# Kernel tuning notes

Hardware: AMD Instinct MI355X
Metric: run time of the kernel (lower is better)

The kernel has to match this reference:

```python
import jax, jax.numpy as jnp
import numpy as np

B, T, IN, H, L, OUT = 1024, 48, 64, 512, 3, 1


def setup_inputs() -> dict:
    key = jax.random.key(0)
    ks = jax.random.split(key, 12)
    s = 0.05
    inp = {
        "x": jax.random.normal(ks[0], (B, T, IN), dtype=jnp.float32),
        # layer 0: input IN -> H ; gates concatenated [f,i,c,o] along last dim
        "Wx0": jax.random.normal(ks[1], (IN, 4 * H), dtype=jnp.float32) * s,
        "Wh0": jax.random.normal(ks[2], (H, 4 * H), dtype=jnp.float32) * s,
        "b0": jnp.zeros((4 * H,), dtype=jnp.float32),
        "Wx1": jax.random.normal(ks[3], (H, 4 * H), dtype=jnp.float32) * s,
        "Wh1": jax.random.normal(ks[4], (H, 4 * H), dtype=jnp.float32) * s,
        "b1": jnp.zeros((4 * H,), dtype=jnp.float32),
        "Wx2": jax.random.normal(ks[5], (H, 4 * H), dtype=jnp.float32) * s,
        "Wh2": jax.random.normal(ks[6], (H, 4 * H), dtype=jnp.float32) * s,
        "b2": jnp.zeros((4 * H,), dtype=jnp.float32),
        "fc_w": jax.random.normal(ks[7], (H, OUT), dtype=jnp.float32) * s,
        "fc_b": jnp.zeros((OUT,), dtype=jnp.float32),
    }
    return inp


def _lstm_cell(Wx, Wh, b, x_t, h, C):
    # fused 4-gate GEMM, same math as 8 separate Linears in the torch code
    g = x_t @ Wx + h @ Wh + b  # [B, 4H]
    f, i, c, o = jnp.split(g, 4, axis=-1)
    f = jax.nn.sigmoid(f)
    i = jax.nn.sigmoid(i)
    c = jnp.tanh(c)
    o = jax.nn.sigmoid(o)
    C_new = f * C + i * c
    h_new = o * jnp.tanh(C_new)  # dropout is identity in eval mode
    return h_new, C_new


def reference(x, Wx0, Wh0, b0, Wx1, Wh1, b1, Wx2, Wh2, b2, fc_w, fc_b):
    params = [(Wx0, Wh0, b0), (Wx1, Wh1, b1), (Wx2, Wh2, b2)]
    Bsz = x.shape[0]
    Hsz = Wh0.shape[0]
    h0 = jnp.zeros((L, Bsz, Hsz), dtype=x.dtype)
    C0 = jnp.zeros((L, Bsz, Hsz), dtype=x.dtype)

    def step(carry, x_t):
        h, C = carry
        inp = x_t
        hs, Cs = [], []
        for l in range(L):
            Wx, Wh, b = params[l]
            hn, Cn = _lstm_cell(Wx, Wh, b, inp, h[l], C[l])
            hs.append(hn)
            Cs.append(Cn)
            inp = hn
        return (jnp.stack(hs), jnp.stack(Cs)), None

    (h, C), _ = jax.lax.scan(step, (h0, C0), jnp.swapaxes(x, 0, 1))
    return h[-1] @ fc_w + fc_b  # [B, OUT]
```

## Files before the change

kernel.cpp:

```cpp
#include <hip/hip_runtime.h>
#include <hip/hip_bf16.h>
#include <stdint.h>

#define BSZ 1024
#define HSZ 512
#define TSZ 48
#define INSZ 64
#define GSZ 2048

typedef __attribute__((ext_vector_type(8))) short bf16x8;
typedef __attribute__((ext_vector_type(4))) float f32x4;

#define GLDS16(g, l)                                                        \
    __builtin_amdgcn_global_load_lds(                                       \
        (const __attribute__((address_space(1))) void*)(g),                 \
        (__attribute__((address_space(3))) void*)(l), 16, 0, 0)

__device__ __forceinline__ float sigmf(float x) { return 1.0f / (1.0f + __expf(-x)); }
__device__ __forceinline__ float tanhf_(float x) { return 2.0f / (1.0f + __expf(-2.0f * x)) - 1.0f; }

__global__ __launch_bounds__(256, 3) void lstm_diag(
    const __hip_bfloat16* __restrict__ xth, const __hip_bfloat16* __restrict__ xtl,
    __hip_bfloat16* __restrict__ hbuf,
    float* __restrict__ Cbuf,
    const __hip_bfloat16* __restrict__ W0h, const __hip_bfloat16* __restrict__ W0l,
    const __hip_bfloat16* __restrict__ W1h, const __hip_bfloat16* __restrict__ W1l,
    const __hip_bfloat16* __restrict__ W2h, const __hip_bfloat16* __restrict__ W2l,
    const float* __restrict__ b0, const float* __restrict__ b1,
    const float* __restrict__ b2,
    int d, int lmin)
{
    __shared__ __align__(16) char lds[49152];

    const int l = lmin + blockIdx.z;
    const int t = d - l;
    const size_t slab = (size_t)BSZ * HSZ;
    __hip_bfloat16* hb = hbuf;
    auto Hb = [&](int par, int ll, int hilo) {
        return hb + (((size_t)par * 3 + ll) * 2 + hilo) * slab;
    };

    const __hip_bfloat16* Wth = (l == 0) ? W0h : (l == 1) ? W1h : W2h;
    const __hip_bfloat16* Wtl = (l == 0) ? W0l : (l == 1) ? W1l : W2l;
    const float* bias = (l == 0) ? b0 : (l == 1) ? b1 : b2;
    const int Kx   = (l == 0) ? INSZ : HSZ;
    const int Ktot = Kx + HSZ;
    const int cur = t & 1, prv = cur ^ 1;
    const __hip_bfloat16* Axh = (l == 0) ? xth + (size_t)t * BSZ * INSZ : Hb(cur, l - 1, 0);
    const __hip_bfloat16* Axl = (l == 0) ? xtl + (size_t)t * BSZ * INSZ : Hb(cur, l - 1, 1);
    const int ldax = Kx;
    const __hip_bfloat16* Ahh = Hb(prv, l, 0);
    const __hip_bfloat16* Ahl = Hb(prv, l, 1);
    float* C = Cbuf + (size_t)l * slab;
    __hip_bfloat16* hhi = Hb(cur, l, 0);
    __hip_bfloat16* hlo = Hb(cur, l, 1);

    const int bid = blockIdx.x + (blockIdx.y << 4);
    const int swz = (bid & 7) * 32 + (bid >> 3);
    const int m0 = (swz & 15) * 64;
    const int n0 = (swz >> 4) * 128;

    const int tid = threadIdx.x;
    const int lane = tid & 63;
    const int wv = tid >> 6;
    const int lrow = lane & 15;
    const int lk = lane >> 4;

    int offA[4][2], offB[2][2];
#pragma unroll
    for (int m = 0; m < 4; ++m) {
        int row = m * 16 + lrow;
#pragma unroll
        for (int kk = 0; kk < 2; ++kk)
            offA[m][kk] = (row * 128 + (lk + kk * 4) * 16) ^ ((row & 7) << 4);
    }
#pragma unroll
    for (int j = 0; j < 2; ++j) {
        int n = wv * 32 + j * 16 + lrow;
#pragma unroll
        for (int kk = 0; kk < 2; ++kk)
            offB[j][kk] = (n * 128 + (lk + kk * 4) * 16) ^ ((n & 7) << 4);
    }

    int rowA[2], ksA[2];
#pragma unroll
    for (int i = 0; i < 2; ++i) {
        int seg = (wv * 2 + i) * 64 + lane;
        rowA[i] = seg >> 3;
        ksA[i] = ((seg & 7) ^ (rowA[i] & 7)) * 8;
    }
    int rowB[4], ksB[4];
#pragma unroll
    for (int i = 0; i < 4; ++i) {
        int seg = (wv * 4 + i) * 64 + lane;
        rowB[i] = seg >> 3;
        ksB[i] = ((seg & 7) ^ (rowB[i] & 7)) * 8;
    }

    char* ldsAh = lds;
    char* ldsAl = lds + 8192;
    char* ldsBh = lds + 16384;
    char* ldsBl = lds + 32768;

    f32x4 acc[4][2];
#pragma unroll
    for (int m = 0; m < 4; ++m)
#pragma unroll
        for (int j = 0; j < 2; ++j) acc[m][j] = (f32x4){0.f, 0.f, 0.f, 0.f};

    auto kstep = [&](const __hip_bfloat16* Ah_, const __hip_bfloat16* Al_, int ldA,
                     int kA, int kW) {
        __syncthreads();
#pragma unroll
        for (int i = 0; i < 2; ++i) {
            size_t ro = (size_t)(m0 + rowA[i]) * ldA + kA + ksA[i];
            GLDS16(Ah_ + ro, ldsAh + (wv * 2 + i) * 1024);
            GLDS16(Al_ + ro, ldsAl + (wv * 2 + i) * 1024);
        }
#pragma unroll
        for (int i = 0; i < 4; ++i) {
            size_t ro = (size_t)(n0 + rowB[i]) * Ktot + kW + ksB[i];
            GLDS16(Wth + ro, ldsBh + (wv * 4 + i) * 1024);
            GLDS16(Wtl + ro, ldsBl + (wv * 4 + i) * 1024);
        }
        __syncthreads();
#pragma unroll
        for (int kk = 0; kk < 2; ++kk) {
            bf16x8 a_h[4], a_l[4], b_h[2], b_l[2];
#pragma unroll
            for (int m = 0; m < 4; ++m) {
                a_h[m] = *(const bf16x8*)(ldsAh + offA[m][kk]);
                a_l[m] = *(const bf16x8*)(ldsAl + offA[m][kk]);
            }
#pragma unroll
            for (int j = 0; j < 2; ++j) {
                b_h[j] = *(const bf16x8*)(ldsBh + offB[j][kk]);
                b_l[j] = *(const bf16x8*)(ldsBl + offB[j][kk]);
            }
#pragma unroll
            for (int m = 0; m < 4; ++m)
#pragma unroll
                for (int j = 0; j < 2; ++j) {
                    acc[m][j] = __builtin_amdgcn_mfma_f32_16x16x32_bf16(a_h[m], b_h[j], acc[m][j], 0, 0, 0);
                    acc[m][j] = __builtin_amdgcn_mfma_f32_16x16x32_bf16(a_l[m], b_h[j], acc[m][j], 0, 0, 0);
                    acc[m][j] = __builtin_amdgcn_mfma_f32_16x16x32_bf16(a_h[m], b_l[j], acc[m][j], 0, 0, 0);
                }
        }
    };

#pragma unroll 1
    for (int k0 = 0; k0 < Kx; k0 += 64) kstep(Axh, Axl, ldax, k0, k0);
#pragma unroll 1
    for (int k0 = 0; k0 < HSZ; k0 += 64) kstep(Ahh, Ahl, HSZ, k0, Kx + k0);

    __syncthreads();
    float* gt = (float*)lds;
#pragma unroll
    for (int m = 0; m < 4; ++m)
#pragma unroll
        for (int j = 0; j < 2; ++j) {
            int col = wv * 32 + j * 16 + lrow;
            int rb = m * 16 + lk * 4;
#pragma unroll
            for (int r = 0; r < 4; ++r) gt[(rb + r) * 132 + col] = acc[m][j][r];
        }
    __syncthreads();

    const int n_l = tid & 31;
    const int rb2 = (tid >> 5) * 8;
    const int n_g = (n0 >> 2) + n_l;
    const float bf = bias[n_g], bi = bias[HSZ + n_g];
    const float bc = bias[2 * HSZ + n_g], bo = bias[3 * HSZ + n_g];
#pragma unroll
    for (int r = 0; r < 8; ++r) {
        int row = rb2 + r;
        int rg = m0 + row;
        float4 g4 = *(const float4*)&gt[row * 132 + n_l * 4];
        float f = sigmf(g4.x + bf);
        float i_ = sigmf(g4.y + bi);
        float c_ = tanhf_(g4.z + bc);
        float o_ = sigmf(g4.w + bo);
        size_t idx = (size_t)rg * HSZ + n_g;
        float Cn = f * C[idx] + i_ * c_;
        C[idx] = Cn;
        float hv = o_ * tanhf_(Cn);
        __hip_bfloat16 hh = __float2bfloat16(hv);
        hhi[idx] = hh;
        hlo[idx] = __float2bfloat16(hv - __bfloat162float(hh));
    }
}

__global__ __launch_bounds__(256) void convert_x(const float* __restrict__ x,
                                                 __hip_bfloat16* __restrict__ xh,
                                                 __hip_bfloat16* __restrict__ xl)
{
    int idx = blockIdx.x * 256 + threadIdx.x;
    int i4 = idx & 15;
    int bt = idx >> 4;
    int t = bt % TSZ;
    int b = bt / TSZ;
    float4 v = *(const float4*)(x + ((size_t)b * TSZ + t) * INSZ + i4 * 4);
    size_t o = ((size_t)t * BSZ + b) * INSZ + i4 * 4;
    float vv[4] = {v.x, v.y, v.z, v.w};
#pragma unroll
    for (int j = 0; j < 4; ++j) {
        __hip_bfloat16 h = __float2bfloat16(vv[j]);
        xh[o + j] = h;
        xl[o + j] = __float2bfloat16(vv[j] - __bfloat162float(h));
    }
}

__global__ __launch_bounds__(256) void convert_w(
    const float* __restrict__ Wx, const float* __restrict__ Wh, int Kx, int Ktot,
    __hip_bfloat16* __restrict__ outh, __hip_bfloat16* __restrict__ outl)
{
    __shared__ float tile[64][65];
    int k0 = blockIdx.x * 64;
    int c0 = blockIdx.y * 64;
    int nb = c0 >> 2;
    const float* src;
    int krel;
    if (k0 < Kx) { src = Wx; krel = k0; } else { src = Wh; krel = k0 - Kx; }
#pragma unroll
    for (int i = 0; i < 16; ++i) {
        int idx = threadIdx.x + i * 256;
        int k_l = idx >> 6, c_l = idx & 63;
        int g = c_l >> 4, n_l = c_l & 15;
        tile[k_l][n_l * 4 + g] = src[(size_t)(krel + k_l) * GSZ + g * HSZ + nb + n_l];
    }
    __syncthreads();
#pragma unroll
    for (int i = 0; i < 16; ++i) {
        int idx = threadIdx.x + i * 256;
        int r_l = idx >> 6, k_l = idx & 63;
        float v = tile[k_l][r_l];
        __hip_bfloat16 h = __float2bfloat16(v);
        size_t o = (size_t)(c0 + r_l) * Ktot + k0 + k_l;
        outh[o] = h;
        outl[o] = __float2bfloat16(v - __bfloat162float(h));
    }
}

__global__ __launch_bounds__(256) void fc_kernel(
    const __hip_bfloat16* __restrict__ hh, const __hip_bfloat16* __restrict__ hl,
    const float* __restrict__ w, const float* __restrict__ b, float* __restrict__ out)
{
    int wave = (blockIdx.x * 256 + threadIdx.x) >> 6;
    int lane = threadIdx.x & 63;
    if (wave >= BSZ) return;
    float s = 0.0f;
#pragma unroll
    for (int k = lane; k < HSZ; k += 64)
        s += (__bfloat162float(hh[wave * HSZ + k]) + __bfloat162float(hl[wave * HSZ + k])) * w[k];
#pragma unroll
    for (int off = 32; off; off >>= 1) s += __shfl_down(s, off);
    if (lane == 0) out[wave] = s + b[0];
}

extern "C" void kernel_launch(void* const* d_in, const int* in_sizes, int n_in,
                              void* d_out, int out_size, void* d_ws, size_t ws_size,
                              hipStream_t stream) {
    const float* x   = (const float*)d_in[0];
    const float* Wx0 = (const float*)d_in[1];
    const float* Wh0 = (const float*)d_in[2];
    const float* b0  = (const float*)d_in[3];
    const float* Wx1 = (const float*)d_in[4];
    const float* Wh1 = (const float*)d_in[5];
    const float* b1  = (const float*)d_in[6];
    const float* Wx2 = (const float*)d_in[7];
    const float* Wh2 = (const float*)d_in[8];
    const float* b2  = (const float*)d_in[9];
    const float* fcw = (const float*)d_in[10];
    const float* fcb = (const float*)d_in[11];

    char* p = (char*)d_ws;
    const size_t hslab = (size_t)BSZ * HSZ * sizeof(__hip_bfloat16);
    __hip_bfloat16* hbuf = (__hip_bfloat16*)p;
    p += 12 * hslab;
    float* Cbuf = (float*)p;
    p += 3 * (size_t)BSZ * HSZ * sizeof(float);
    const size_t zero_bytes = (size_t)(p - (char*)d_ws);

    const size_t xslab = (size_t)TSZ * BSZ * INSZ * sizeof(__hip_bfloat16);
    __hip_bfloat16* xth = (__hip_bfloat16*)p; p += xslab;
    __hip_bfloat16* xtl = (__hip_bfloat16*)p; p += xslab;

    const int K0 = INSZ + HSZ;
    const int K12 = 2 * HSZ;
    const size_t w0s = (size_t)GSZ * K0 * sizeof(__hip_bfloat16);
    const size_t w12s = (size_t)GSZ * K12 * sizeof(__hip_bfloat16);
    __hip_bfloat16* w0h = (__hip_bfloat16*)p; p += w0s;
    __hip_bfloat16* w0l = (__hip_bfloat16*)p; p += w0s;
    __hip_bfloat16* w1h = (__hip_bfloat16*)p; p += w12s;
    __hip_bfloat16* w1l = (__hip_bfloat16*)p; p += w12s;
    __hip_bfloat16* w2h = (__hip_bfloat16*)p; p += w12s;
    __hip_bfloat16* w2l = (__hip_bfloat16*)p; p += w12s;

    hipMemsetAsync(d_ws, 0, zero_bytes, stream);

    convert_x<<<dim3(BSZ * TSZ * 16 / 256), dim3(256), 0, stream>>>(x, xth, xtl);
    convert_w<<<dim3(K0 / 64, GSZ / 64), dim3(256), 0, stream>>>(Wx0, Wh0, INSZ, K0, w0h, w0l);
    convert_w<<<dim3(K12 / 64, GSZ / 64), dim3(256), 0, stream>>>(Wx1, Wh1, HSZ, K12, w1h, w1l);
    convert_w<<<dim3(K12 / 64, GSZ / 64), dim3(256), 0, stream>>>(Wx2, Wh2, HSZ, K12, w2h, w2l);

    for (int dgn = 0; dgn < TSZ + 2; ++dgn) {
        int lmin = (dgn - (TSZ - 1)) > 0 ? (dgn - (TSZ - 1)) : 0;
        int lmax = dgn < 2 ? dgn : 2;
        int ncells = lmax - lmin + 1;
        lstm_diag<<<dim3(16, 16, ncells), dim3(256), 0, stream>>>(
            xth, xtl, hbuf, Cbuf,
            w0h, w0l, w1h, w1l, w2h, w2l,
            b0, b1, b2, dgn, lmin);
    }

    __hip_bfloat16* h2h = hbuf + (((size_t)1 * 3 + 2) * 2 + 0) * BSZ * HSZ;
    __hip_bfloat16* h2l = hbuf + (((size_t)1 * 3 + 2) * 2 + 1) * BSZ * HSZ;
    fc_kernel<<<dim3(BSZ / 4), dim3(256), 0, stream>>>(h2h, h2l, fcw, fcb, (float*)d_out);
}
```

Before: 1.869 ms.

## Double-buffer activation tiles in LDS and load weights directly into registers

```diff
diff --git a/kernel.cpp b/kernel.cpp
--- a/kernel.cpp
+++ b/kernel.cpp
@@ -30,14 +30,13 @@
     const float* __restrict__ b2,
     int d, int lmin)
 {
-    __shared__ __align__(16) char lds[49152];
+    __shared__ __align__(16) char lds[33792];
 
     const int l = lmin + blockIdx.z;
     const int t = d - l;
     const size_t slab = (size_t)BSZ * HSZ;
-    __hip_bfloat16* hb = hbuf;
     auto Hb = [&](int par, int ll, int hilo) {
-        return hb + (((size_t)par * 3 + ll) * 2 + hilo) * slab;
+        return hbuf + (((size_t)par * 3 + ll) * 2 + hilo) * slab;
     };
 
     const __hip_bfloat16* Wth = (l == 0) ? W0h : (l == 1) ? W1h : W2h;
@@ -45,10 +44,11 @@
     const float* bias = (l == 0) ? b0 : (l == 1) ? b1 : b2;
     const int Kx   = (l == 0) ? INSZ : HSZ;
     const int Ktot = Kx + HSZ;
+    const int nkx  = Kx >> 6;
+    const int nkt  = Ktot >> 6;
     const int cur = t & 1, prv = cur ^ 1;
     const __hip_bfloat16* Axh = (l == 0) ? xth + (size_t)t * BSZ * INSZ : Hb(cur, l - 1, 0);
     const __hip_bfloat16* Axl = (l == 0) ? xtl + (size_t)t * BSZ * INSZ : Hb(cur, l - 1, 1);
-    const int ldax = Kx;
     const __hip_bfloat16* Ahh = Hb(prv, l, 0);
     const __hip_bfloat16* Ahl = Hb(prv, l, 1);
     float* C = Cbuf + (size_t)l * slab;
@@ -66,20 +66,13 @@
     const int lrow = lane & 15;
     const int lk = lane >> 4;
 
-    int offA[4][2], offB[2][2];
+    int offA[4][2];
 #pragma unroll
     for (int m = 0; m < 4; ++m) {
         int row = m * 16 + lrow;
 #pragma unroll
         for (int kk = 0; kk < 2; ++kk)
             offA[m][kk] = (row * 128 + (lk + kk * 4) * 16) ^ ((row & 7) << 4);
-    }
-#pragma unroll
-    for (int j = 0; j < 2; ++j) {
-        int n = wv * 32 + j * 16 + lrow;
-#pragma unroll
-        for (int kk = 0; kk < 2; ++kk)
-            offB[j][kk] = (n * 128 + (lk + kk * 4) * 16) ^ ((n & 7) << 4);
     }
 
     int rowA[2], ksA[2];
@@ -89,18 +82,11 @@
         rowA[i] = seg >> 3;
         ksA[i] = ((seg & 7) ^ (rowA[i] & 7)) * 8;
     }
-    int rowB[4], ksB[4];
-#pragma unroll
-    for (int i = 0; i < 4; ++i) {
-        int seg = (wv * 4 + i) * 64 + lane;
-        rowB[i] = seg >> 3;
-        ksB[i] = ((seg & 7) ^ (rowB[i] & 7)) * 8;
-    }
-
-    char* ldsAh = lds;
-    char* ldsAl = lds + 8192;
-    char* ldsBh = lds + 16384;
-    char* ldsBl = lds + 32768;
+
+    const int bcol = n0 + wv * 32 + lrow;
+    const __hip_bfloat16* pB0h = Wth + (size_t)bcol * Ktot + lk * 8;
+    const __hip_bfloat16* pB0l = Wtl + (size_t)bcol * Ktot + lk * 8;
+    const size_t jstride = (size_t)16 * Ktot;
 
     f32x4 acc[4][2];
 #pragma unroll
@@ -108,52 +94,65 @@
 #pragma unroll
         for (int j = 0; j < 2; ++j) acc[m][j] = (f32x4){0.f, 0.f, 0.f, 0.f};
 
-    auto kstep = [&](const __hip_bfloat16* Ah_, const __hip_bfloat16* Al_, int ldA,
-                     int kA, int kW) {
-        __syncthreads();
+    auto stage = [&](int ks, int buf) {
+        const __hip_bfloat16* sh;
+        const __hip_bfloat16* sl;
+        int ldA, krel;
+        if (ks < nkx) { sh = Axh; sl = Axl; ldA = Kx; krel = ks * 64; }
+        else          { sh = Ahh; sl = Ahl; ldA = HSZ; krel = (ks - nkx) * 64; }
+        char* dh = lds + buf * 16384;
+        char* dl = dh + 8192;
 #pragma unroll
         for (int i = 0; i < 2; ++i) {
-            size_t ro = (size_t)(m0 + rowA[i]) * ldA + kA + ksA[i];
-            GLDS16(Ah_ + ro, ldsAh + (wv * 2 + i) * 1024);
-            GLDS16(Al_ + ro, ldsAl + (wv * 2 + i) * 1024);
+            size_t ro = (size_t)(m0 + rowA[i]) * ldA + krel + ksA[i];
+            GLDS16(sh + ro, dh + (wv * 2 + i) * 1024);
+            GLDS16(sl + ro, dl + (wv * 2 + i) * 1024);
         }
-#pragma unroll
-        for (int i = 0; i < 4; ++i) {
-            size_t ro = (size_t)(n0 + rowB[i]) * Ktot + kW + ksB[i];
-            GLDS16(Wth + ro, ldsBh + (wv * 4 + i) * 1024);
-            GLDS16(Wtl + ro, ldsBl + (wv * 4 + i) * 1024);
-        }
-        __syncthreads();
+    };
+
+    stage(0, 0);
+    __syncthreads();
+
+#pragma unroll 1
+    for (int ks = 0; ks < nkt; ++ks) {
+        const int buf = ks & 1;
+        if (ks + 1 < nkt) stage(ks + 1, buf ^ 1);
+
+        bf16x8 bh[2][2], bl[2][2];
+        const __hip_bfloat16* ph = pB0h + ks * 64;
+        const __hip_bfloat16* pl = pB0l + ks * 64;
+#pragma unroll
+        for (int j = 0; j < 2; ++j)
+#pragma unroll
+            for (int kk = 0; kk < 2; ++kk) {
+                bh[j][kk] = *(const bf16x8*)(ph + j * jstride + kk * 32);
+                bl[j][kk] = *(const bf16x8*)(pl + j * jstride + kk * 32);
+            }
+
+        char* ah_base = lds + buf * 16384;
+        char* al_base = ah_base + 8192;
+        __builtin_amdgcn_s_setprio(1);
 #pragma unroll
         for (int kk = 0; kk < 2; ++kk) {
-            bf16x8 a_h[4], a_l[4], b_h[2], b_l[2];
+            bf16x8 a_h[4], a_l[4];
 #pragma unroll
             for (int m = 0; m < 4; ++m) {
-                a_h[m] = *(const bf16x8*)(ldsAh + offA[m][kk]);
-                a_l[m] = *(const bf16x8*)(ldsAl + offA[m][kk]);
+                a_h[m] = *(const bf16x8*)(ah_base + offA[m][kk]);
+                a_l[m] = *(const bf16x8*)(al_base + offA[m][kk]);
             }
 #pragma unroll
-            for (int j = 0; j < 2; ++j) {
-                b_h[j] = *(const bf16x8*)(ldsBh + offB[j][kk]);
-                b_l[j] = *(const bf16x8*)(ldsBl + offB[j][kk]);
-            }
-#pragma unroll
             for (int m = 0; m < 4; ++m)
 #pragma unroll
                 for (int j = 0; j < 2; ++j) {
-                    acc[m][j] = __builtin_amdgcn_mfma_f32_16x16x32_bf16(a_h[m], b_h[j], acc[m][j], 0, 0, 0);
-                    acc[m][j] = __builtin_amdgcn_mfma_f32_16x16x32_bf16(a_l[m], b_h[j], acc[m][j], 0, 0, 0);
-                    acc[m][j] = __builtin_amdgcn_mfma_f32_16x16x32_bf16(a_h[m], b_l[j], acc[m][j], 0, 0, 0);
+                    acc[m][j] = __builtin_amdgcn_mfma_f32_16x16x32_bf16(a_h[m], bh[j][kk], acc[m][j], 0, 0, 0);
+                    acc[m][j] = __builtin_amdgcn_mfma_f32_16x16x32_bf16(a_l[m], bh[j][kk], acc[m][j], 0, 0, 0);
+                    acc[m][j] = __builtin_amdgcn_mfma_f32_16x16x32_bf16(a_h[m], bl[j][kk], acc[m][j], 0, 0, 0);
                 }
         }
-    };
-
-#pragma unroll 1
-    for (int k0 = 0; k0 < Kx; k0 += 64) kstep(Axh, Axl, ldax, k0, k0);
-#pragma unroll 1
-    for (int k0 = 0; k0 < HSZ; k0 += 64) kstep(Ahh, Ahl, HSZ, k0, Kx + k0);
-
-    __syncthreads();
+        __builtin_amdgcn_s_setprio(0);
+        __syncthreads();
+    }
+
     float* gt = (float*)lds;
 #pragma unroll
     for (int m = 0; m < 4; ++m)
```

After: 2.498 ms. 33.7% more time.

## Pre-tile operands into MFMA-ready chunk layout and switch to 32x32x16 MFMA

Applied to the files above, without the earlier changes.

```diff
diff --git a/kernel.cpp b/kernel.cpp
--- a/kernel.cpp
+++ b/kernel.cpp
@@ -9,7 +9,7 @@
 #define GSZ 2048
 
 typedef __attribute__((ext_vector_type(8))) short bf16x8;
-typedef __attribute__((ext_vector_type(4))) float f32x4;
+typedef __attribute__((ext_vector_type(16))) float f32x16;
 
 #define GLDS16(g, l)                                                        \
     __builtin_amdgcn_global_load_lds(                                       \
@@ -31,24 +31,30 @@
     int d, int lmin)
 {
     __shared__ __align__(16) char lds[49152];
+    char* ldsAh = lds;
+    char* ldsAl = lds + 8192;
+    char* ldsBh = lds + 16384;
+    char* ldsBl = lds + 32768;
 
     const int l = lmin + blockIdx.z;
     const int t = d - l;
     const size_t slab = (size_t)BSZ * HSZ;
-    __hip_bfloat16* hb = hbuf;
     auto Hb = [&](int par, int ll, int hilo) {
-        return hb + (((size_t)par * 3 + ll) * 2 + hilo) * slab;
+        return hbuf + (((size_t)par * 3 + ll) * 2 + hilo) * slab;
     };
 
     const __hip_bfloat16* Wth = (l == 0) ? W0h : (l == 1) ? W1h : W2h;
     const __hip_bfloat16* Wtl = (l == 0) ? W0l : (l == 1) ? W1l : W2l;
     const float* bias = (l == 0) ? b0 : (l == 1) ? b1 : b2;
     const int Kx   = (l == 0) ? INSZ : HSZ;
+    const int KCax = (l == 0) ? 8 : 64;
     const int Ktot = Kx + HSZ;
+    const int KCt  = Ktot >> 3;
+    const int nkx  = Kx >> 6;
+    const int nkt  = Ktot >> 6;
     const int cur = t & 1, prv = cur ^ 1;
     const __hip_bfloat16* Axh = (l == 0) ? xth + (size_t)t * BSZ * INSZ : Hb(cur, l - 1, 0);
     const __hip_bfloat16* Axl = (l == 0) ? xtl + (size_t)t * BSZ * INSZ : Hb(cur, l - 1, 1);
-    const int ldax = Kx;
     const __hip_bfloat16* Ahh = Hb(prv, l, 0);
     const __hip_bfloat16* Ahl = Hb(prv, l, 1);
     float* C = Cbuf + (size_t)l * slab;
@@ -59,116 +65,87 @@
     const int swz = (bid & 7) * 32 + (bid >> 3);
     const int m0 = (swz & 15) * 64;
     const int n0 = (swz >> 4) * 128;
+    const int p  = swz & 15;
+    const int np = swz >> 4;
 
     const int tid = threadIdx.x;
     const int lane = tid & 63;
     const int wv = tid >> 6;
-    const int lrow = lane & 15;
-    const int lk = lane >> 4;
-
-    int offA[4][2], offB[2][2];
-#pragma unroll
-    for (int m = 0; m < 4; ++m) {
-        int row = m * 16 + lrow;
-#pragma unroll
-        for (int kk = 0; kk < 2; ++kk)
-            offA[m][kk] = (row * 128 + (lk + kk * 4) * 16) ^ ((row & 7) << 4);
-    }
-#pragma unroll
-    for (int j = 0; j < 2; ++j) {
-        int n = wv * 32 + j * 16 + lrow;
-#pragma unroll
-        for (int kk = 0; kk < 2; ++kk)
-            offB[j][kk] = (n * 128 + (lk + kk * 4) * 16) ^ ((n & 7) << 4);
-    }
-
-    int rowA[2], ksA[2];
-#pragma unroll
-    for (int i = 0; i < 2; ++i) {
-        int seg = (wv * 2 + i) * 64 + lane;
-        rowA[i] = seg >> 3;
-        ksA[i] = ((seg & 7) ^ (rowA[i] & 7)) * 8;
-    }
-    int rowB[4], ksB[4];
-#pragma unroll
-    for (int i = 0; i < 4; ++i) {
-        int seg = (wv * 4 + i) * 64 + lane;
-        rowB[i] = seg >> 3;
-        ksB[i] = ((seg & 7) ^ (rowB[i] & 7)) * 8;
-    }
-
-    char* ldsAh = lds;
-    char* ldsAl = lds + 8192;
-    char* ldsBh = lds + 16384;
-    char* ldsBl = lds + 32768;
-
-    f32x4 acc[4][2];
-#pragma unroll
-    for (int m = 0; m < 4; ++m)
-#pragma unroll
-        for (int j = 0; j < 2; ++j) acc[m][j] = (f32x4){0.f, 0.f, 0.f, 0.f};
-
-    auto kstep = [&](const __hip_bfloat16* Ah_, const __hip_bfloat16* Al_, int ldA,
-                     int kA, int kW) {
-        __syncthreads();
+    const int lrow32 = lane & 31;
+    const int lk2 = lane >> 5;
+
+    int offA[2][4], offB[4];
+#pragma unroll
+    for (int mf = 0; mf < 2; ++mf)
+#pragma unroll
+        for (int ks = 0; ks < 4; ++ks)
+            offA[mf][ks] = (ks * 2 + lk2) * 1024 + (mf * 32 + lrow32) * 16;
+#pragma unroll
+    for (int ks = 0; ks < 4; ++ks)
+        offB[ks] = (ks * 2 + lk2) * 2048 + (wv * 32 + lrow32) * 16;
+
+    f32x16 acc[2];
+#pragma unroll
+    for (int mf = 0; mf < 2; ++mf)
+#pragma unroll
+        for (int r = 0; r < 16; ++r) acc[mf][r] = 0.0f;
+
+    auto stage = [&](const __hip_bfloat16* sh, const __hip_bfloat16* sl,
+                     int KCa, int kcA0, int kcW0) {
 #pragma unroll
         for (int i = 0; i < 2; ++i) {
-            size_t ro = (size_t)(m0 + rowA[i]) * ldA + kA + ksA[i];
-            GLDS16(Ah_ + ro, ldsAh + (wv * 2 + i) * 1024);
-            GLDS16(Al_ + ro, ldsAl + (wv * 2 + i) * 1024);
+            int sa = wv * 2 + i;
+            size_t ro = ((size_t)p * KCa + kcA0 + sa) * 512 + lane * 8;
+            GLDS16(sh + ro, ldsAh + sa * 1024);
+            GLDS16(sl + ro, ldsAl + sa * 1024);
         }
 #pragma unroll
         for (int i = 0; i < 4; ++i) {
-            size_t ro = (size_t)(n0 + rowB[i]) * Ktot + kW + ksB[i];
-            GLDS16(Wth + ro, ldsBh + (wv * 4 + i) * 1024);
-            GLDS16(Wtl + ro, ldsBl + (wv * 4 + i) * 1024);
-        }
-        __syncthreads();
-#pragma unroll
-        for (int kk = 0; kk < 2; ++kk) {
-            bf16x8 a_h[4], a_l[4], b_h[2], b_l[2];
-#pragma unroll
-            for (int m = 0; m < 4; ++m) {
-                a_h[m] = *(const bf16x8*)(ldsAh + offA[m][kk]);
-                a_l[m] = *(const bf16x8*)(ldsAl + offA[m][kk]);
-            }
-#pragma unroll
-            for (int j = 0; j < 2; ++j) {
-                b_h[j] = *(const bf16x8*)(ldsBh + offB[j][kk]);
-                b_l[j] = *(const bf16x8*)(ldsBl + offB[j][kk]);
-            }
-#pragma unroll
-            for (int m = 0; m < 4; ++m)
-#pragma unroll
-                for (int j = 0; j < 2; ++j) {
-                    acc[m][j] = __builtin_amdgcn_mfma_f32_16x16x32_bf16(a_h[m], b_h[j], acc[m][j], 0, 0, 0);
-                    acc[m][j] = __builtin_amdgcn_mfma_f32_16x16x32_bf16(a_l[m], b_h[j], acc[m][j], 0, 0, 0);
-                    acc[m][j] = __builtin_amdgcn_mfma_f32_16x16x32_bf16(a_h[m], b_l[j], acc[m][j], 0, 0, 0);
-                }
+            int sb = wv * 4 + i;
+            size_t ro = ((size_t)np * KCt + kcW0 + (sb >> 1)) * 1024 + (sb & 1) * 512 + lane * 8;
+            GLDS16(Wth + ro, ldsBh + sb * 1024);
+            GLDS16(Wtl + ro, ldsBl + sb * 1024);
         }
     };
 
 #pragma unroll 1
-    for (int k0 = 0; k0 < Kx; k0 += 64) kstep(Axh, Axl, ldax, k0, k0);
-#pragma unroll 1
-    for (int k0 = 0; k0 < HSZ; k0 += 64) kstep(Ahh, Ahl, HSZ, k0, Kx + k0);
+    for (int ks = 0; ks < nkt; ++ks) {
+        __syncthreads();
+        if (ks < nkx) stage(Axh, Axl, KCax, ks * 8, ks * 8);
+        else          stage(Ahh, Ahl, 64, (ks - nkx) * 8, ks * 8);
+        __syncthreads();
+#pragma unroll
+        for (int ksub = 0; ksub < 4; ++ksub) {
+            bf16x8 ah0 = *(const bf16x8*)(ldsAh + offA[0][ksub]);
+            bf16x8 ah1 = *(const bf16x8*)(ldsAh + offA[1][ksub]);
+            bf16x8 al0 = *(const bf16x8*)(ldsAl + offA[0][ksub]);
+            bf16x8 al1 = *(const bf16x8*)(ldsAl + offA[1][ksub]);
+            bf16x8 bh  = *(const bf16x8*)(ldsBh + offB[ksub]);
+            bf16x8 bl  = *(const bf16x8*)(ldsBl + offB[ksub]);
+            acc[0] = __builtin_amdgcn_mfma_f32_32x32x16_bf16(ah0, bh, acc[0], 0, 0, 0);
+            acc[1] = __builtin_amdgcn_mfma_f32_32x32x16_bf16(ah1, bh, acc[1], 0, 0, 0);
+            acc[0] = __builtin_amdgcn_mfma_f32_32x32x16_bf16(al0, bh, acc[0], 0, 0, 0);
+            acc[1] = __builtin_amdgcn_mfma_f32_32x32x16_bf16(al1, bh, acc[1], 0, 0, 0);
+            acc[0] = __builtin_amdgcn_mfma_f32_32x32x16_bf16(ah0, bl, acc[0], 0, 0, 0);
+            acc[1] = __builtin_amdgcn_mfma_f32_32x32x16_bf16(ah1, bl, acc[1], 0, 0, 0);
+        }
+    }
 
     __syncthreads();
     float* gt = (float*)lds;
 #pragma unroll
-    for (int m = 0; m < 4; ++m)
-#pragma unroll
-        for (int j = 0; j < 2; ++j) {
-            int col = wv * 32 + j * 16 + lrow;
-            int rb = m * 16 + lk * 4;
-#pragma unroll
-            for (int r = 0; r < 4; ++r) gt[(rb + r) * 132 + col] = acc[m][j][r];
+    for (int mf = 0; mf < 2; ++mf)
+#pragma unroll
+        for (int rg = 0; rg < 16; ++rg) {
+            int row = mf * 32 + (rg & 3) + 8 * (rg >> 2) + 4 * lk2;
+            gt[row * 132 + wv * 32 + lrow32] = acc[mf][rg];
         }
     __syncthreads();
 
     const int n_l = tid & 31;
     const int rb2 = (tid >> 5) * 8;
     const int n_g = (n0 >> 2) + n_l;
+    const int kc_h = n_g >> 3, e_h = n_g & 7;
     const float bf = bias[n_g], bi = bias[HSZ + n_g];
     const float bc = bias[2 * HSZ + n_g], bo = bias[3 * HSZ + n_g];
 #pragma unroll
@@ -180,13 +157,14 @@
         float i_ = sigmf(g4.y + bi);
         float c_ = tanhf_(g4.z + bc);
         float o_ = sigmf(g4.w + bo);
-        size_t idx = (size_t)rg * HSZ + n_g;
-        float Cn = f * C[idx] + i_ * c_;
-        C[idx] = Cn;
+        size_t cidx = (size_t)rg * HSZ + n_g;
+        float Cn = f * C[cidx] + i_ * c_;
+        C[cidx] = Cn;
         float hv = o_ * tanhf_(Cn);
         __hip_bfloat16 hh = __float2bfloat16(hv);
-        hhi[idx] = hh;
-        hlo[idx] = __float2bfloat16(hv - __bfloat162float(hh));
+        size_t hidx = (((size_t)(rg >> 6) * 64 + kc_h) * 64 + (rg & 63)) * 8 + e_h;
+        hhi[hidx] = hh;
+        hlo[hidx] = __float2bfloat16(hv - __bfloat162float(hh));
     }
 }
 
@@ -194,50 +172,54 @@
                                                  __hip_bfloat16* __restrict__ xh,
                                                  __hip_bfloat16* __restrict__ xl)
 {
-    int idx = blockIdx.x * 256 + threadIdx.x;
-    int i4 = idx & 15;
-    int bt = idx >> 4;
-    int t = bt % TSZ;
-    int b = bt / TSZ;
-    float4 v = *(const float4*)(x + ((size_t)b * TSZ + t) * INSZ + i4 * 4);
-    size_t o = ((size_t)t * BSZ + b) * INSZ + i4 * 4;
-    float vv[4] = {v.x, v.y, v.z, v.w};
-#pragma unroll
-    for (int j = 0; j < 4; ++j) {
-        __hip_bfloat16 h = __float2bfloat16(vv[j]);
-        xh[o + j] = h;
-        xl[o + j] = __float2bfloat16(vv[j] - __bfloat162float(h));
-    }
+    int gid = blockIdx.x * 256 + threadIdx.x;
+    int kc = gid & 7;
+    int rem = gid >> 3;
+    int r = rem & 63; rem >>= 6;
+    int pp = rem & 15;
+    int t = rem >> 4;
+    int b = pp * 64 + r;
+    const float* src = x + ((size_t)b * TSZ + t) * INSZ + kc * 8;
+    short hi8[8], lo8[8];
+#pragma unroll
+    for (int e = 0; e < 8; ++e) {
+        float v = src[e];
+        __hip_bfloat16 h = __float2bfloat16(v);
+        hi8[e] = *(short*)&h;
+        __hip_bfloat16 lo = __float2bfloat16(v - __bfloat162float(h));
+        lo8[e] = *(short*)&lo;
+    }
+    size_t o = ((((size_t)t * 16 + pp) * 8 + kc) * 64 + r) * 8;
+    *(bf16x8*)((__hip_bfloat16*)xh + o) = *(bf16x8*)hi8;
+    *(bf16x8*)((__hip_bfloat16*)xl + o) = *(bf16x8*)lo8;
 }
 
 __global__ __launch_bounds__(256) void convert_w(
     const float* __restrict__ Wx, const float* __restrict__ Wh, int Kx, int Ktot,
     __hip_bfloat16* __restrict__ outh, __hip_bfloat16* __restrict__ outl)
 {
-    __shared__ float tile[64][65];
-    int k0 = blockIdx.x * 64;
-    int c0 = blockIdx.y * 64;
-    int nb = c0 >> 2;
+    __shared__ float tile[64][129];
+    const int kt = blockIdx.x, np = blockIdx.y;
+    const int k0 = kt * 64;
     const float* src;
     int krel;
     if (k0 < Kx) { src = Wx; krel = k0; } else { src = Wh; krel = k0 - Kx; }
 #pragma unroll
-    for (int i = 0; i < 16; ++i) {
+    for (int i = 0; i < 32; ++i) {
         int idx = threadIdx.x + i * 256;
-        int k_l = idx >> 6, c_l = idx & 63;
-        int g = c_l >> 4, n_l = c_l & 15;
-        tile[k_l][n_l * 4 + g] = src[(size_t)(krel + k_l) * GSZ + g * HSZ + nb + n_l];
+        int k_l = idx >> 7, gate = (idx >> 5) & 3, n_l = idx & 31;
+        tile[k_l][n_l * 4 + gate] = src[(size_t)(krel + k_l) * GSZ + gate * HSZ + np * 32 + n_l];
     }
     __syncthreads();
-#pragma unroll
-    for (int i = 0; i < 16; ++i) {
+    const size_t obase = ((size_t)np * (Ktot >> 3) + kt * 8) * 1024;
+#pragma unroll
+    for (int i = 0; i < 32; ++i) {
         int idx = threadIdx.x + i * 256;
-        int r_l = idx >> 6, k_l = idx & 63;
-        float v = tile[k_l][r_l];
+        int kcl = idx >> 10, c = (idx >> 3) & 127, e = idx & 7;
+        float v = tile[kcl * 8 + e][c];
         __hip_bfloat16 h = __float2bfloat16(v);
-        size_t o = (size_t)(c0 + r_l) * Ktot + k0 + k_l;
-        outh[o] = h;
-        outl[o] = __float2bfloat16(v - __bfloat162float(h));
+        outh[obase + idx] = h;
+        outl[obase + idx] = __float2bfloat16(v - __bfloat162float(h));
     }
 }
 
@@ -248,10 +230,18 @@
     int wave = (blockIdx.x * 256 + threadIdx.x) >> 6;
     int lane = threadIdx.x & 63;
     if (wave >= BSZ) return;
+    int pp = wave >> 6, r = wave & 63;
+    size_t o = (((size_t)pp * 64 + lane) * 64 + r) * 8;
+    bf16x8 vh = *(const bf16x8*)(hh + o);
+    bf16x8 vl = *(const bf16x8*)(hl + o);
     float s = 0.0f;
 #pragma unroll
-    for (int k = lane; k < HSZ; k += 64)
-        s += (__bfloat162float(hh[wave * HSZ + k]) + __bfloat162float(hl[wave * HSZ + k])) * w[k];
+    for (int e = 0; e < 8; ++e) {
+        ushort uh = (ushort)vh[e], ul = (ushort)vl[e];
+        __hip_bfloat16 bh = *(__hip_bfloat16*)&uh;
+        __hip_bfloat16 bl = *(__hip_bfloat16*)&ul;
+        s += (__bfloat162float(bh) + __bfloat162float(bl)) * w[lane * 8 + e];
+    }
 #pragma unroll
     for (int off = 32; off; off >>= 1) s += __shfl_down(s, off);
     if (lane == 0) out[wave] = s + b[0];
@@ -298,10 +288,10 @@
 
     hipMemsetAsync(d_ws, 0, zero_bytes, stream);
 
-    convert_x<<<dim3(BSZ * TSZ * 16 / 256), dim3(256), 0, stream>>>(x, xth, xtl);
-    convert_w<<<dim3(K0 / 64, GSZ / 64), dim3(256), 0, stream>>>(Wx0, Wh0, INSZ, K0, w0h, w0l);
-    convert_w<<<dim3(K12 / 64, GSZ / 64), dim3(256), 0, stream>>>(Wx1, Wh1, HSZ, K12, w1h, w1l);
-    convert_w<<<dim3(K12 / 64, GSZ / 64), dim3(256), 0, stream>>>(Wx2, Wh2, HSZ, K12, w2h, w2l);
+    convert_x<<<dim3(TSZ * BSZ * 8 / 256), dim3(256), 0, stream>>>(x, xth, xtl);
+    convert_w<<<dim3(K0 / 64, 16), dim3(256), 0, stream>>>(Wx0, Wh0, INSZ, K0, w0h, w0l);
+    convert_w<<<dim3(K12 / 64, 16), dim3(256), 0, stream>>>(Wx1, Wh1, HSZ, K12, w1h, w1l);
+    convert_w<<<dim3(K12 / 64, 16), dim3(256), 0, stream>>>(Wx2, Wh2, HSZ, K12, w2h, w2l);
 
     for (int dgn = 0; dgn < TSZ + 2; ++dgn) {
         int lmin = (dgn - (TSZ - 1)) > 0 ? (dgn - (TSZ - 1)) : 0;
```

After: 2.042 ms. +9.3%, slower.
